# Kernel optimization log

Measured on AMD Instinct MI355X. Metric: run time of the kernel, lower is better.

## Reference

```python
import jax, jax.numpy as jnp
import numpy as np

N, C_F, C_C = 4, 128, 256
H_IMG, W_IMG = 480, 640
HF, WF = H_IMG // 2, W_IMG // 2          # fine feature map 240x320
K, STRIDE, PAD = 5, 4, 2                 # fine_window_size, hw0_f//hw0_c, W//2
WW = K * K                               # 25
L = (H_IMG // 8) * (W_IMG // 8)          # 4800 coarse cells
M = 5000                                 # number of matches
VIEW = (-1, H_IMG * K * 2, WW, W_IMG * K // WW)  # (-1, 4800, 25, 128), exactly the torch .view


def _unfold(x):
    """torch.nn.functional.unfold(x, (K,K), stride=STRIDE, padding=PAD).
    x: [N, C, H, W] -> [N, C*K*K, Ho*Wo] with torch channel ordering (c, kh, kw)."""
    n, c, h, w = x.shape
    xp = jnp.pad(x, ((0, 0), (0, 0), (PAD, PAD), (PAD, PAD)))
    ho = (h + 2 * PAD - K) // STRIDE + 1
    wo = (w + 2 * PAD - K) // STRIDE + 1
    ii = (jnp.arange(ho) * STRIDE)[:, None] + jnp.arange(K)[None, :]  # [Ho, K]
    jj = (jnp.arange(wo) * STRIDE)[:, None] + jnp.arange(K)[None, :]  # [Wo, K]
    p = xp[:, :, ii][:, :, :, :, jj]          # [N, C, Ho, K, Wo, K]
    p = p.transpose(0, 1, 3, 5, 2, 4)          # [N, C, K, K, Ho, Wo]
    return p.reshape(n, c * K * K, ho * wo)


def setup_inputs() -> dict:
    key = jax.random.key(0)
    ks = jax.random.split(key, 11)
    feat_f0 = jax.random.normal(ks[0], (N, C_F, HF, WF), jnp.float32)
    feat_f1 = jax.random.normal(ks[1], (N, C_F, HF, WF), jnp.float32)
    feat_c0 = jax.random.normal(ks[2], (N, L, C_C), jnp.float32)
    feat_c1 = jax.random.normal(ks[3], (N, L, C_C), jnp.float32)
    b_ids = jax.random.randint(ks[4], (M,), 0, N)
    i_ids = jax.random.randint(ks[5], (M,), 0, L)
    j_ids = jax.random.randint(ks[6], (M,), 0, L)
    # kaiming_normal fan_out, relu: std = sqrt(2 / fan_out) with fan_out = out_features
    down_proj_w = jax.random.normal(ks[7], (C_F, C_C), jnp.float32) * np.sqrt(2.0 / C_F)
    down_proj_b = jnp.zeros((C_F,), jnp.float32)
    merge_w = jax.random.normal(ks[8], (C_F, 2 * C_F), jnp.float32) * np.sqrt(2.0 / C_F)
    merge_b = jnp.zeros((C_F,), jnp.float32)
    return {"feat_f0": feat_f0, "feat_f1": feat_f1, "feat_c0": feat_c0, "feat_c1": feat_c1,
            "b_ids": b_ids, "i_ids": i_ids, "j_ids": j_ids,
            "down_proj_w": down_proj_w, "down_proj_b": down_proj_b,
            "merge_w": merge_w, "merge_b": merge_b}


def reference(feat_f0, feat_f1, feat_c0, feat_c1, b_ids, i_ids, j_ids,
              down_proj_w, down_proj_b, merge_w, merge_b):
    # dense unfold (im2col) then faithful memory-reinterpreting .view
    u0 = _unfold(feat_f0).reshape(VIEW)            # [N, 4800, 25, 128]
    u1 = _unfold(feat_f1).reshape(VIEW)
    # sparse window gather
    f0 = u0[b_ids, i_ids]                          # [M, WW, C_F]
    f1 = u1[b_ids, j_ids]                          # [M, WW, C_F]
    # cat_c_feat branch: down-project coarse feats and merge
    c_win = jnp.concatenate([feat_c0[b_ids, i_ids], feat_c1[b_ids, j_ids]], axis=0)  # [2M, C_C]
    c_win = c_win @ down_proj_w.T + down_proj_b                                      # [2M, C_F]
    f = jnp.concatenate([f0, f1], axis=0)                                            # [2M, WW, C_F]
    c_rep = jnp.broadcast_to(c_win[:, None, :], (f.shape[0], WW, C_F))               # [2M, WW, C_F]
    merged = jnp.concatenate([f, c_rep], axis=-1) @ merge_w.T + merge_b              # [2M, WW, C_F]
    return merged[:M], merged[M:]
```

## Files before the change

kernel.cpp:

```cpp
#include <hip/hip_runtime.h>
#include <hip/hip_bf16.h>

#define MM 5000
#define LC 4800

typedef __attribute__((ext_vector_type(8))) short bf16x8;
typedef __attribute__((ext_vector_type(4))) float f32x4;

__device__ __forceinline__ unsigned short f2bf(float f) {
    unsigned int u = __builtin_bit_cast(unsigned int, f);
    u += 0x7fffu + ((u >> 16) & 1u);
    return (unsigned short)(u >> 16);
}

__global__ void k0_prep(const float* __restrict__ merge_w,
                        const float* __restrict__ down_w,
                        const float* __restrict__ merge_b,
                        const float* __restrict__ down_b,
                        unsigned short* __restrict__ w1_bf,
                        unsigned short* __restrict__ wc_bf,
                        float* __restrict__ bvec)
{
    int o = blockIdx.x * 256 + threadIdx.x;
    int cf = o >> 8, cc = o & 255;
    const float* w2row = merge_w + cf * 256 + 128;
    float acc = 0.f;
    #pragma unroll 4
    for (int j = 0; j < 128; ++j)
        acc = fmaf(w2row[j], down_w[j * 256 + cc], acc);
    wc_bf[o] = f2bf(acc);
    if (o < 16384)
        w1_bf[o] = f2bf(merge_w[(o >> 7) * 256 + (o & 127)]);
    if (o < 128) {
        const float* w2r = merge_w + o * 256 + 128;
        float a = merge_b[o];
        for (int j = 0; j < 128; ++j) a = fmaf(down_b[j], w2r[j], a);
        bvec[o] = a;
    }
}

__global__ void __launch_bounds__(256) k1_bias(
    const float* __restrict__ feat_c0, const float* __restrict__ feat_c1,
    const int* __restrict__ b_ids, const int* __restrict__ i_ids,
    const int* __restrict__ j_ids,
    const unsigned short* __restrict__ wc_bf, const float* __restrict__ bvec,
    float* __restrict__ bias2)
{
    __shared__ unsigned short ac[32][264];
    const int t = threadIdx.x;
    const int base = blockIdx.x * 32;
    {
        int row = t >> 3;
        int seg = (t & 7) * 32;
        int sm = base + row; if (sm > 2 * MM - 1) sm = 2 * MM - 1;
        int side = sm >= MM;
        int mm = sm - side * MM;
        int id = side ? j_ids[mm] : i_ids[mm];
        int b  = b_ids[mm];
        const float* src = (side ? feat_c1 : feat_c0)
                           + (size_t)(b * LC + id) * 256 + seg;
        const float4* s4 = (const float4*)src;
        #pragma unroll
        for (int i = 0; i < 8; ++i) {
            float4 v = s4[i];
            ushort4 u; u.x = f2bf(v.x); u.y = f2bf(v.y); u.z = f2bf(v.z); u.w = f2bf(v.w);
            *(ushort4*)&ac[row][seg + i * 4] = u;
        }
    }
    __syncthreads();
    const int lane = t & 63, wave = t >> 6;
    const int ln = lane & 15, q = lane >> 4;
    const int n0 = wave * 32;
    f32x4 acc[2][2] = {};
    #pragma unroll
    for (int k0 = 0; k0 < 8; ++k0) {
        bf16x8 a0 = *(const bf16x8*)&ac[ln][k0 * 32 + q * 8];
        bf16x8 a1 = *(const bf16x8*)&ac[16 + ln][k0 * 32 + q * 8];
        bf16x8 b0 = *(const bf16x8*)(wc_bf + (size_t)(n0 + ln) * 256 + k0 * 32 + q * 8);
        bf16x8 b1 = *(const bf16x8*)(wc_bf + (size_t)(n0 + 16 + ln) * 256 + k0 * 32 + q * 8);
        acc[0][0] = __builtin_amdgcn_mfma_f32_16x16x32_bf16(a0, b0, acc[0][0], 0, 0, 0);
        acc[0][1] = __builtin_amdgcn_mfma_f32_16x16x32_bf16(a0, b1, acc[0][1], 0, 0, 0);
        acc[1][0] = __builtin_amdgcn_mfma_f32_16x16x32_bf16(a1, b0, acc[1][0], 0, 0, 0);
        acc[1][1] = __builtin_amdgcn_mfma_f32_16x16x32_bf16(a1, b1, acc[1][1], 0, 0, 0);
    }
    #pragma unroll
    for (int mt = 0; mt < 2; ++mt)
      #pragma unroll
      for (int nt = 0; nt < 2; ++nt) {
        int cf = n0 + nt * 16 + ln;
        float bv = bvec[cf];
        #pragma unroll
        for (int r = 0; r < 4; ++r) {
            int sm = base + mt * 16 + q * 4 + r;
            if (sm < 2 * MM)
                bias2[(size_t)sm * 128 + cf] = acc[mt][nt][r] + bv;
        }
      }
}

__global__ void __launch_bounds__(256, 6) k2_main(
    const float* __restrict__ feat_f0, const float* __restrict__ feat_f1,
    const int* __restrict__ b_ids, const int* __restrict__ i_ids,
    const int* __restrict__ j_ids,
    const unsigned short* __restrict__ w1_bf, const float* __restrict__ bias2,
    float* __restrict__ out)
{
    __shared__ unsigned short fw[32][136];
    __shared__ float brow[128];
    const int t = threadIdx.x;
    const int bx = blockIdx.x;
    const int side = bx >= MM;
    const int m = bx - side * MM;
    const float* feat = side ? feat_f1 : feat_f0;
    const int l = side ? j_ids[m] : i_ids[m];
    const int n = b_ids[m];
    const float* fn = feat + (size_t)n * (128 * 240 * 320);

    if (t < 128) brow[t] = bias2[(size_t)bx * 128 + t];

    const unsigned fbase = (unsigned)l * 3200u;
    const unsigned cc0 = fbase / 4800u;
    const unsigned p0  = fbase - cc0 * 4800u;
    const unsigned rem = 4800u - p0;
    const int split = (int)(rem < 3200u ? rem : 3200u);
    const unsigned cc1 = cc0 + 1u;
    const int ch0 = (int)(cc0 / 25u), k50 = (int)(cc0 - (unsigned)ch0 * 25u);
    const int kh0 = k50 / 5, kw0 = k50 - kh0 * 5;
    const int ch1 = (int)(cc1 / 25u), k51 = (int)(cc1 - (unsigned)ch1 * 25u);
    const int kh1 = k51 / 5, kw1 = k51 - kh1 * 5;
    const int base0 = ch0 * 76800, base1 = ch1 * 76800;
    const int khm20 = kh0 - 2, khm21 = kh1 - 2;
    const int kwm20 = kw0 - 2, kwm21 = kw1 - 2;

    float val[13];
    unsigned int vmask = 0;
    #pragma unroll
    for (int it = 0; it < 13; ++it) {
        int idx = t + it * 256;
        idx = idx < 3199 ? idx : 3199;
        const int selB = idx >= split;
        const unsigned p = (unsigned)(selB ? idx - split : idx + (int)p0);
        const int ho = (int)(p / 80u);
        const int wo = (int)p - ho * 80;
        const int r   = 4 * ho + (selB ? khm21 : khm20);
        const int col = 4 * wo + (selB ? kwm21 : kwm20);
        const int ok = (r >= 0) & (col >= 0);
        int off = (selB ? base1 : base0) + r * 320 + col;
        off = ok ? off : 0;
        val[it] = fn[off];
        vmask |= (unsigned)ok << it;
    }

    const int lane = t & 63, wave = t >> 6;
    const int ln = lane & 15, q = lane >> 4;
    const int n0 = wave * 32;
    bf16x8 bf[2][4];
    #pragma unroll
    for (int nt = 0; nt < 2; ++nt)
      #pragma unroll
      for (int k0 = 0; k0 < 4; ++k0)
        bf[nt][k0] = *(const bf16x8*)(w1_bf + (n0 + nt * 16 + ln) * 128 + k0 * 32 + q * 8);

    #pragma unroll
    for (int it = 0; it < 13; ++it) {
        int idx = t + it * 256;
        if (it < 12 || idx < 3200) {
            float v = ((vmask >> it) & 1u) ? val[it] : 0.f;
            fw[idx >> 7][idx & 127] = f2bf(v);
        }
    }
    __syncthreads();

    f32x4 acc[2][2] = {};
    #pragma unroll
    for (int k0 = 0; k0 < 4; ++k0) {
        bf16x8 a0 = *(const bf16x8*)&fw[ln][k0 * 32 + q * 8];
        bf16x8 a1 = *(const bf16x8*)&fw[16 + ln][k0 * 32 + q * 8];
        acc[0][0] = __builtin_amdgcn_mfma_f32_16x16x32_bf16(a0, bf[0][k0], acc[0][0], 0, 0, 0);
        acc[0][1] = __builtin_amdgcn_mfma_f32_16x16x32_bf16(a0, bf[1][k0], acc[0][1], 0, 0, 0);
        acc[1][0] = __builtin_amdgcn_mfma_f32_16x16x32_bf16(a1, bf[0][k0], acc[1][0], 0, 0, 0);
        acc[1][1] = __builtin_amdgcn_mfma_f32_16x16x32_bf16(a1, bf[1][k0], acc[1][1], 0, 0, 0);
    }
    float* ob = out + (size_t)bx * 3200;
    #pragma unroll
    for (int nt = 0; nt < 2; ++nt) {
        int cf = n0 + nt * 16 + ln;
        float bv = brow[cf];
        #pragma unroll
        for (int mt = 0; mt < 2; ++mt)
          #pragma unroll
          for (int r = 0; r < 4; ++r) {
            int w = mt * 16 + q * 4 + r;
            if (w < 25)
                ob[w * 128 + cf] = acc[mt][nt][r] + bv;
          }
    }
}

extern "C" void kernel_launch(void* const* d_in, const int* in_sizes, int n_in,
                              void* d_out, int out_size, void* d_ws, size_t ws_size,
                              hipStream_t stream) {
    const float* feat_f0 = (const float*)d_in[0];
    const float* feat_f1 = (const float*)d_in[1];
    const float* feat_c0 = (const float*)d_in[2];
    const float* feat_c1 = (const float*)d_in[3];
    const int*   b_ids   = (const int*)d_in[4];
    const int*   i_ids   = (const int*)d_in[5];
    const int*   j_ids   = (const int*)d_in[6];
    const float* down_w  = (const float*)d_in[7];
    const float* down_b  = (const float*)d_in[8];
    const float* merge_w = (const float*)d_in[9];
    const float* merge_b = (const float*)d_in[10];
    float* out = (float*)d_out;

    char* ws = (char*)d_ws;
    unsigned short* w1_bf = (unsigned short*)(ws);
    unsigned short* wc_bf = (unsigned short*)(ws + 32768);
    float* bvec  = (float*)(ws + 98304);
    float* bias2 = (float*)(ws + 98816);

    hipLaunchKernelGGL(k0_prep, dim3(128), dim3(256), 0, stream,
                       merge_w, down_w, merge_b, down_b, w1_bf, wc_bf, bvec);
    hipLaunchKernelGGL(k1_bias, dim3((2 * MM + 31) / 32), dim3(256), 0, stream,
                       feat_c0, feat_c1, b_ids, i_ids, j_ids, wc_bf, bvec, bias2);
    hipLaunchKernelGGL(k2_main, dim3(2 * MM), dim3(256), 0, stream,
                       feat_f0, feat_f1, b_ids, i_ids, j_ids, w1_bf, bias2, out);
}
```

Baseline: 429.2 us.

## Sort matches by window key and remap block order for cache locality

```diff
diff --git a/kernel.cpp b/kernel.cpp
--- a/kernel.cpp
+++ b/kernel.cpp
@@ -3,6 +3,7 @@
 
 #define MM 5000
 #define LC 4800
+#define NB 38400
 
 typedef __attribute__((ext_vector_type(8))) short bf16x8;
 typedef __attribute__((ext_vector_type(4))) float f32x4;
@@ -19,9 +20,12 @@
                         const float* __restrict__ down_b,
                         unsigned short* __restrict__ w1_bf,
                         unsigned short* __restrict__ wc_bf,
-                        float* __restrict__ bvec)
+                        float* __restrict__ bvec,
+                        unsigned int* __restrict__ hist)
 {
     int o = blockIdx.x * 256 + threadIdx.x;
+    if (o < NB) hist[o] = 0u;
+    if (o + 32768 < NB) hist[o + 32768] = 0u;
     int cf = o >> 8, cc = o & 255;
     const float* w2row = merge_w + cf * 256 + 128;
     float acc = 0.f;
@@ -36,6 +40,64 @@
         float a = merge_b[o];
         for (int j = 0; j < 128; ++j) a = fmaf(down_b[j], w2r[j], a);
         bvec[o] = a;
+    }
+}
+
+__device__ __forceinline__ unsigned sort_key(int s, const int* b_ids,
+                                             const int* i_ids, const int* j_ids) {
+    int side = s >= MM;
+    int mm = s - side * MM;
+    int l = side ? j_ids[mm] : i_ids[mm];
+    return (unsigned)(side * (4 * LC) + b_ids[mm] * LC + l);
+}
+
+__global__ void k_hist(const int* __restrict__ b_ids, const int* __restrict__ i_ids,
+                       const int* __restrict__ j_ids, unsigned int* __restrict__ hist)
+{
+    int s = blockIdx.x * 256 + threadIdx.x;
+    if (s < 2 * MM)
+        atomicAdd(&hist[sort_key(s, b_ids, i_ids, j_ids)], 1u);
+}
+
+__global__ void __launch_bounds__(1024) k_scan(unsigned int* __restrict__ hist)
+{
+    __shared__ unsigned part[1024];
+    const int t = threadIdx.x;
+    const int CH = (NB + 1023) / 1024;
+    const int s0 = t * CH;
+    unsigned loc[CH];
+    unsigned sum = 0;
+    #pragma unroll
+    for (int i = 0; i < CH; ++i) {
+        int idx = s0 + i;
+        unsigned v = (idx < NB) ? hist[idx] : 0u;
+        loc[i] = sum;
+        sum += v;
+    }
+    part[t] = sum;
+    __syncthreads();
+    for (int off = 1; off < 1024; off <<= 1) {
+        unsigned v = (t >= off) ? part[t - off] : 0u;
+        __syncthreads();
+        part[t] += v;
+        __syncthreads();
+    }
+    unsigned base = (t == 0) ? 0u : part[t - 1];
+    #pragma unroll
+    for (int i = 0; i < CH; ++i) {
+        int idx = s0 + i;
+        if (idx < NB) hist[idx] = base + loc[i];
+    }
+}
+
+__global__ void k_scatter(const int* __restrict__ b_ids, const int* __restrict__ i_ids,
+                          const int* __restrict__ j_ids, unsigned int* __restrict__ hist,
+                          int* __restrict__ perm)
+{
+    int s = blockIdx.x * 256 + threadIdx.x;
+    if (s < 2 * MM) {
+        unsigned pos = atomicAdd(&hist[sort_key(s, b_ids, i_ids, j_ids)], 1u);
+        perm[pos] = s;
     }
 }
 
@@ -103,12 +165,14 @@
     const int* __restrict__ b_ids, const int* __restrict__ i_ids,
     const int* __restrict__ j_ids,
     const unsigned short* __restrict__ w1_bf, const float* __restrict__ bias2,
+    const int* __restrict__ perm,
     float* __restrict__ out)
 {
     __shared__ unsigned short fw[32][136];
     __shared__ float brow[128];
     const int t = threadIdx.x;
-    const int bx = blockIdx.x;
+    const int bid = blockIdx.x;
+    const int bx = perm[(bid & 7) * 1250 + (bid >> 3)];
     const int side = bx >= MM;
     const int m = bx - side * MM;
     const float* feat = side ? feat_f1 : feat_f0;
@@ -218,11 +282,18 @@
     unsigned short* wc_bf = (unsigned short*)(ws + 32768);
     float* bvec  = (float*)(ws + 98304);
     float* bias2 = (float*)(ws + 98816);
+    int*   perm  = (int*)(ws + 5218816);
+    unsigned int* hist = (unsigned int*)(ws + 5258816);
 
     hipLaunchKernelGGL(k0_prep, dim3(128), dim3(256), 0, stream,
-                       merge_w, down_w, merge_b, down_b, w1_bf, wc_bf, bvec);
+                       merge_w, down_w, merge_b, down_b, w1_bf, wc_bf, bvec, hist);
+    hipLaunchKernelGGL(k_hist, dim3(40), dim3(256), 0, stream,
+                       b_ids, i_ids, j_ids, hist);
+    hipLaunchKernelGGL(k_scan, dim3(1), dim3(1024), 0, stream, hist);
+    hipLaunchKernelGGL(k_scatter, dim3(40), dim3(256), 0, stream,
+                       b_ids, i_ids, j_ids, hist, perm);
     hipLaunchKernelGGL(k1_bias, dim3((2 * MM + 31) / 32), dim3(256), 0, stream,
                        feat_c0, feat_c1, b_ids, i_ids, j_ids, wc_bf, bvec, bias2);
     hipLaunchKernelGGL(k2_main, dim3(2 * MM), dim3(256), 0, stream,
-                       feat_f0, feat_f1, b_ids, i_ids, j_ids, w1_bf, bias2, out);
-}
+                       feat_f0, feat_f1, b_ids, i_ids, j_ids, w1_bf, bias2, perm, out);
+}
```

Measured after the change: 461.4 us. 1.07x slower.

## Sort matches by window key to improve gather locality; stage stores through LDS

Applied to the files above, without the earlier changes.

```diff
diff --git a/kernel.cpp b/kernel.cpp
--- a/kernel.cpp
+++ b/kernel.cpp
@@ -36,6 +36,61 @@
         float a = merge_b[o];
         for (int j = 0; j < 128; ++j) a = fmaf(down_b[j], w2r[j], a);
         bvec[o] = a;
+    }
+}
+
+__global__ void __launch_bounds__(1024) k_sort(
+    const int* __restrict__ b_ids, const int* __restrict__ i_ids,
+    const int* __restrict__ j_ids, int* __restrict__ perm)
+{
+    __shared__ unsigned hist[4800];
+    __shared__ unsigned part[1024];
+    const int t = threadIdx.x;
+    for (int i = t; i < 4800; i += 1024) hist[i] = 0u;
+    __syncthreads();
+    unsigned key[10];
+    #pragma unroll
+    for (int i = 0; i < 10; ++i) {
+        int s = t + i * 1024;
+        if (s < 2 * MM) {
+            int side = s >= MM;
+            int mm = s - side * MM;
+            int l = side ? j_ids[mm] : i_ids[mm];
+            key[i] = (unsigned)(side * (4 * LC) + b_ids[mm] * LC + l) >> 3;
+            atomicAdd(&hist[key[i]], 1u);
+        } else key[i] = 0u;
+    }
+    __syncthreads();
+    unsigned loc[5], sum = 0u;
+    #pragma unroll
+    for (int i = 0; i < 5; ++i) {
+        int idx = t * 5 + i;
+        unsigned v = (idx < 4800) ? hist[idx] : 0u;
+        loc[i] = sum; sum += v;
+    }
+    part[t] = sum;
+    __syncthreads();
+    for (int off = 1; off < 1024; off <<= 1) {
+        unsigned v = (t >= off) ? part[t - off] : 0u;
+        __syncthreads();
+        part[t] += v;
+        __syncthreads();
+    }
+    unsigned base = (t == 0) ? 0u : part[t - 1];
+    __syncthreads();
+    #pragma unroll
+    for (int i = 0; i < 5; ++i) {
+        int idx = t * 5 + i;
+        if (idx < 4800) hist[idx] = base + loc[i];
+    }
+    __syncthreads();
+    #pragma unroll
+    for (int i = 0; i < 10; ++i) {
+        int s = t + i * 1024;
+        if (s < 2 * MM) {
+            unsigned pos = atomicAdd(&hist[key[i]], 1u);
+            perm[pos] = s;
+        }
     }
 }
 
@@ -98,17 +153,22 @@
       }
 }
 
-__global__ void __launch_bounds__(256, 6) k2_main(
+__global__ void __launch_bounds__(256, 8) k2_main(
     const float* __restrict__ feat_f0, const float* __restrict__ feat_f1,
     const int* __restrict__ b_ids, const int* __restrict__ i_ids,
     const int* __restrict__ j_ids,
     const unsigned short* __restrict__ w1_bf, const float* __restrict__ bias2,
+    const int* __restrict__ perm,
     float* __restrict__ out)
 {
-    __shared__ unsigned short fw[32][136];
-    __shared__ float brow[128];
+    __shared__ char smem[12800];
+    unsigned short (*fw)[136] = (unsigned short (*)[136])smem;
+    float* brow = (float*)(smem + 8704);
+    float* dls  = (float*)smem;
+
     const int t = threadIdx.x;
-    const int bx = blockIdx.x;
+    const int bid = blockIdx.x;
+    const int bx = perm[(bid & 7) * 1250 + (bid >> 3)];
     const int side = bx >= MM;
     const int m = bx - side * MM;
     const float* feat = side ? feat_f1 : feat_f0;
@@ -171,6 +231,9 @@
     }
     __syncthreads();
 
+    const float bv0 = brow[n0 + ln];
+    const float bv1 = brow[n0 + 16 + ln];
+
     f32x4 acc[2][2] = {};
     #pragma unroll
     for (int k0 = 0; k0 < 4; ++k0) {
@@ -181,20 +244,28 @@
         acc[1][0] = __builtin_amdgcn_mfma_f32_16x16x32_bf16(a1, bf[0][k0], acc[1][0], 0, 0, 0);
         acc[1][1] = __builtin_amdgcn_mfma_f32_16x16x32_bf16(a1, bf[1][k0], acc[1][1], 0, 0, 0);
     }
-    float* ob = out + (size_t)bx * 3200;
+    __syncthreads();
+
     #pragma unroll
     for (int nt = 0; nt < 2; ++nt) {
         int cf = n0 + nt * 16 + ln;
-        float bv = brow[cf];
+        float bv = nt ? bv1 : bv0;
         #pragma unroll
         for (int mt = 0; mt < 2; ++mt)
           #pragma unroll
           for (int r = 0; r < 4; ++r) {
             int w = mt * 16 + q * 4 + r;
             if (w < 25)
-                ob[w * 128 + cf] = acc[mt][nt][r] + bv;
+                dls[w * 128 + cf] = acc[mt][nt][r] + bv;
           }
     }
+    __syncthreads();
+
+    float4* ob4 = (float4*)(out + (size_t)bx * 3200);
+    const float4* d4 = (const float4*)dls;
+    #pragma unroll
+    for (int i = t; i < 800; i += 256)
+        ob4[i] = d4[i];
 }
 
 extern "C" void kernel_launch(void* const* d_in, const int* in_sizes, int n_in,
@@ -218,11 +289,14 @@
     unsigned short* wc_bf = (unsigned short*)(ws + 32768);
     float* bvec  = (float*)(ws + 98304);
     float* bias2 = (float*)(ws + 98816);
+    int*   perm  = (int*)(ws + 5218816);
 
     hipLaunchKernelGGL(k0_prep, dim3(128), dim3(256), 0, stream,
                        merge_w, down_w, merge_b, down_b, w1_bf, wc_bf, bvec);
+    hipLaunchKernelGGL(k_sort, dim3(1), dim3(1024), 0, stream,
+                       b_ids, i_ids, j_ids, perm);
     hipLaunchKernelGGL(k1_bias, dim3((2 * MM + 31) / 32), dim3(256), 0, stream,
                        feat_c0, feat_c1, b_ids, i_ids, j_ids, wc_bf, bvec, bias2);
     hipLaunchKernelGGL(k2_main, dim3(2 * MM), dim3(256), 0, stream,
-                       feat_f0, feat_f1, b_ids, i_ids, j_ids, w1_bf, bias2, out);
-}
+                       feat_f0, feat_f1, b_ids, i_ids, j_ids, w1_bf, bias2, perm, out);
+}
```

New measurement: 430.1 us. Within noise of the previous version (+0.2%).

## Sort window gathers by location and pair them per block with duplicate reuse

Applied to the files above, without the earlier changes.

```diff
diff --git a/kernel.cpp b/kernel.cpp
--- a/kernel.cpp
+++ b/kernel.cpp
@@ -44,10 +44,55 @@
     const int* __restrict__ b_ids, const int* __restrict__ i_ids,
     const int* __restrict__ j_ids,
     const unsigned short* __restrict__ wc_bf, const float* __restrict__ bvec,
-    float* __restrict__ bias2)
+    float* __restrict__ bias2, int* __restrict__ perm)
 {
-    __shared__ unsigned short ac[32][264];
+    __shared__ unsigned smbuf_u[5056];
     const int t = threadIdx.x;
+
+    if (blockIdx.x == (2 * MM + 31) / 32) {
+        unsigned* hist = smbuf_u;
+        unsigned* part = smbuf_u + 4800;
+        for (int i = t; i < 4800; i += 256) hist[i] = 0u;
+        __syncthreads();
+        for (int s = t; s < 2 * MM; s += 256) {
+            int side = s >= MM; int mm = s - side * MM;
+            int l = side ? j_ids[mm] : i_ids[mm];
+            atomicAdd(&hist[((unsigned)(side * (4 * LC) + b_ids[mm] * LC + l)) >> 3], 1u);
+        }
+        __syncthreads();
+        unsigned loc[19], sum = 0u;
+        const int s0i = t * 19;
+        #pragma unroll
+        for (int i = 0; i < 19; ++i) {
+            int idx = s0i + i;
+            unsigned v = (idx < 4800) ? hist[idx] : 0u;
+            loc[i] = sum; sum += v;
+        }
+        part[t] = sum;
+        __syncthreads();
+        for (int off = 1; off < 256; off <<= 1) {
+            unsigned v = (t >= off) ? part[t - off] : 0u;
+            __syncthreads();
+            part[t] += v;
+            __syncthreads();
+        }
+        unsigned base = (t == 0) ? 0u : part[t - 1];
+        #pragma unroll
+        for (int i = 0; i < 19; ++i) {
+            int idx = s0i + i;
+            if (idx < 4800) hist[idx] = base + loc[i];
+        }
+        __syncthreads();
+        for (int s = t; s < 2 * MM; s += 256) {
+            int side = s >= MM; int mm = s - side * MM;
+            int l = side ? j_ids[mm] : i_ids[mm];
+            unsigned pos = atomicAdd(&hist[((unsigned)(side * (4 * LC) + b_ids[mm] * LC + l)) >> 3], 1u);
+            perm[pos] = s;
+        }
+        return;
+    }
+
+    unsigned short (*ac)[264] = (unsigned short (*)[264])smbuf_u;
     const int base = blockIdx.x * 32;
     {
         int row = t >> 3;
@@ -98,69 +143,51 @@
       }
 }
 
-__global__ void __launch_bounds__(256, 6) k2_main(
-    const float* __restrict__ feat_f0, const float* __restrict__ feat_f1,
-    const int* __restrict__ b_ids, const int* __restrict__ i_ids,
-    const int* __restrict__ j_ids,
-    const unsigned short* __restrict__ w1_bf, const float* __restrict__ bias2,
-    float* __restrict__ out)
-{
-    __shared__ unsigned short fw[32][136];
-    __shared__ float brow[128];
-    const int t = threadIdx.x;
-    const int bx = blockIdx.x;
-    const int side = bx >= MM;
-    const int m = bx - side * MM;
-    const float* feat = side ? feat_f1 : feat_f0;
-    const int l = side ? j_ids[m] : i_ids[m];
-    const int n = b_ids[m];
-    const float* fn = feat + (size_t)n * (128 * 240 * 320);
-
-    if (t < 128) brow[t] = bias2[(size_t)bx * 128 + t];
-
-    const unsigned fbase = (unsigned)l * 3200u;
-    const unsigned cc0 = fbase / 4800u;
-    const unsigned p0  = fbase - cc0 * 4800u;
-    const unsigned rem = 4800u - p0;
-    const int split = (int)(rem < 3200u ? rem : 3200u);
-    const unsigned cc1 = cc0 + 1u;
-    const int ch0 = (int)(cc0 / 25u), k50 = (int)(cc0 - (unsigned)ch0 * 25u);
-    const int kh0 = k50 / 5, kw0 = k50 - kh0 * 5;
-    const int ch1 = (int)(cc1 / 25u), k51 = (int)(cc1 - (unsigned)ch1 * 25u);
-    const int kh1 = k51 / 5, kw1 = k51 - kh1 * 5;
-    const int base0 = ch0 * 76800, base1 = ch1 * 76800;
-    const int khm20 = kh0 - 2, khm21 = kh1 - 2;
-    const int kwm20 = kw0 - 2, kwm21 = kw1 - 2;
-
-    float val[13];
-    unsigned int vmask = 0;
+struct GP { int split, base0, base1, khm20, khm21, kwm20, kwm21, p0; };
+
+__device__ __forceinline__ GP decodeParams(int l) {
+    GP g;
+    unsigned fbase = (unsigned)l * 3200u;
+    unsigned cc0 = fbase / 4800u;
+    unsigned p0 = fbase - cc0 * 4800u;
+    unsigned rem = 4800u - p0;
+    g.split = (int)(rem < 3200u ? rem : 3200u);
+    g.p0 = (int)p0;
+    unsigned cc1 = cc0 + 1u;
+    int ch0 = (int)(cc0 / 25u), k50 = (int)(cc0 - (unsigned)ch0 * 25u);
+    int kh0 = k50 / 5, kw0 = k50 - kh0 * 5;
+    int ch1 = (int)(cc1 / 25u), k51 = (int)(cc1 - (unsigned)ch1 * 25u);
+    int kh1 = k51 / 5, kw1 = k51 - kh1 * 5;
+    g.base0 = ch0 * 76800; g.base1 = ch1 * 76800;
+    g.khm20 = kh0 - 2; g.khm21 = kh1 - 2;
+    g.kwm20 = kw0 - 2; g.kwm21 = kw1 - 2;
+    return g;
+}
+
+__device__ __forceinline__ unsigned gatherIssue(const GP g, const float* __restrict__ fn,
+                                                int t, float val[13]) {
+    unsigned vmask = 0;
     #pragma unroll
     for (int it = 0; it < 13; ++it) {
         int idx = t + it * 256;
         idx = idx < 3199 ? idx : 3199;
-        const int selB = idx >= split;
-        const unsigned p = (unsigned)(selB ? idx - split : idx + (int)p0);
+        const int selB = idx >= g.split;
+        const unsigned p = (unsigned)(selB ? idx - g.split : idx + g.p0);
         const int ho = (int)(p / 80u);
         const int wo = (int)p - ho * 80;
-        const int r   = 4 * ho + (selB ? khm21 : khm20);
-        const int col = 4 * wo + (selB ? kwm21 : kwm20);
+        const int r   = 4 * ho + (selB ? g.khm21 : g.khm20);
+        const int col = 4 * wo + (selB ? g.kwm21 : g.kwm20);
         const int ok = (r >= 0) & (col >= 0);
-        int off = (selB ? base1 : base0) + r * 320 + col;
+        int off = (selB ? g.base1 : g.base0) + r * 320 + col;
         off = ok ? off : 0;
         val[it] = fn[off];
         vmask |= (unsigned)ok << it;
     }
-
-    const int lane = t & 63, wave = t >> 6;
-    const int ln = lane & 15, q = lane >> 4;
-    const int n0 = wave * 32;
-    bf16x8 bf[2][4];
-    #pragma unroll
-    for (int nt = 0; nt < 2; ++nt)
-      #pragma unroll
-      for (int k0 = 0; k0 < 4; ++k0)
-        bf[nt][k0] = *(const bf16x8*)(w1_bf + (n0 + nt * 16 + ln) * 128 + k0 * 32 + q * 8);
-
+    return vmask;
+}
+
+__device__ __forceinline__ void cvtToLds(unsigned short (*fw)[136], int t,
+                                         const float val[13], unsigned vmask) {
     #pragma unroll
     for (int it = 0; it < 13; ++it) {
         int idx = t + it * 256;
@@ -169,9 +196,11 @@
             fw[idx >> 7][idx & 127] = f2bf(v);
         }
     }
-    __syncthreads();
-
-    f32x4 acc[2][2] = {};
+}
+
+__device__ __forceinline__ void mfma22(const unsigned short (*fw)[136],
+                                       const bf16x8 (&bf)[2][4],
+                                       int ln, int q, f32x4 (&acc)[2][2]) {
     #pragma unroll
     for (int k0 = 0; k0 < 4; ++k0) {
         bf16x8 a0 = *(const bf16x8*)&fw[ln][k0 * 32 + q * 8];
@@ -181,6 +210,11 @@
         acc[1][0] = __builtin_amdgcn_mfma_f32_16x16x32_bf16(a1, bf[0][k0], acc[1][0], 0, 0, 0);
         acc[1][1] = __builtin_amdgcn_mfma_f32_16x16x32_bf16(a1, bf[1][k0], acc[1][1], 0, 0, 0);
     }
+}
+
+__device__ __forceinline__ void storeD(const f32x4 (&acc)[2][2], const float* brow,
+                                       float* __restrict__ out, int bx,
+                                       int n0, int ln, int q) {
     float* ob = out + (size_t)bx * 3200;
     #pragma unroll
     for (int nt = 0; nt < 2; ++nt) {
@@ -195,6 +229,76 @@
                 ob[w * 128 + cf] = acc[mt][nt][r] + bv;
           }
     }
+}
+
+__global__ void __launch_bounds__(256, 6) k2_main(
+    const float* __restrict__ feat_f0, const float* __restrict__ feat_f1,
+    const int* __restrict__ b_ids, const int* __restrict__ i_ids,
+    const int* __restrict__ j_ids,
+    const unsigned short* __restrict__ w1_bf, const float* __restrict__ bias2,
+    const int* __restrict__ perm,
+    float* __restrict__ out)
+{
+    __shared__ unsigned short fw0[32][136];
+    __shared__ unsigned short fw1[32][136];
+    __shared__ float brow0[128], brow1[128];
+    const int t = threadIdx.x;
+    const int bid = blockIdx.x;
+    const int qq = (bid & 7) * 625 + (bid >> 3);
+    const int s0 = perm[2 * qq], s1 = perm[2 * qq + 1];
+
+    const int side0 = s0 >= MM, m0 = s0 - side0 * MM;
+    const int l0 = side0 ? j_ids[m0] : i_ids[m0];
+    const int n0b = b_ids[m0];
+    const int side1 = s1 >= MM, m1 = s1 - side1 * MM;
+    const int l1 = side1 ? j_ids[m1] : i_ids[m1];
+    const int n1b = b_ids[m1];
+    const float* fn0 = (side0 ? feat_f1 : feat_f0) + (size_t)n0b * (128 * 240 * 320);
+    const float* fn1 = (side1 ? feat_f1 : feat_f0) + (size_t)n1b * (128 * 240 * 320);
+    const bool dup = (l0 == l1) && (n0b == n1b) && (side0 == side1);
+
+    if (t < 128) {
+        brow0[t] = bias2[(size_t)s0 * 128 + t];
+        brow1[t] = bias2[(size_t)s1 * 128 + t];
+    }
+
+    GP g0 = decodeParams(l0);
+    float val[13];
+    unsigned vm = gatherIssue(g0, fn0, t, val);
+
+    const int lane = t & 63, wave = t >> 6;
+    const int ln = lane & 15, q = lane >> 4;
+    const int n0 = wave * 32;
+    bf16x8 bf[2][4];
+    #pragma unroll
+    for (int nt = 0; nt < 2; ++nt)
+      #pragma unroll
+      for (int k0 = 0; k0 < 4; ++k0)
+        bf[nt][k0] = *(const bf16x8*)(w1_bf + (n0 + nt * 16 + ln) * 128 + k0 * 32 + q * 8);
+
+    cvtToLds(fw0, t, val, vm);
+    __syncthreads();
+
+    unsigned vm1 = 0;
+    if (!dup) {
+        GP g1 = decodeParams(l1);
+        vm1 = gatherIssue(g1, fn1, t, val);
+    }
+
+    f32x4 acc[2][2] = {};
+    mfma22(fw0, bf, ln, q, acc);
+    storeD(acc, brow0, out, s0, n0, ln, q);
+    if (dup) {
+        storeD(acc, brow1, out, s1, n0, ln, q);
+        return;
+    }
+
+    cvtToLds(fw1, t, val, vm1);
+    __syncthreads();
+
+    f32x4 acc1[2][2] = {};
+    mfma22(fw1, bf, ln, q, acc1);
+    storeD(acc1, brow1, out, s1, n0, ln, q);
 }
 
 extern "C" void kernel_launch(void* const* d_in, const int* in_sizes, int n_in,
@@ -218,11 +322,12 @@
     unsigned short* wc_bf = (unsigned short*)(ws + 32768);
     float* bvec  = (float*)(ws + 98304);
     float* bias2 = (float*)(ws + 98816);
+    int*   perm  = (int*)(ws + 5218816);
 
     hipLaunchKernelGGL(k0_prep, dim3(128), dim3(256), 0, stream,
                        merge_w, down_w, merge_b, down_b, w1_bf, wc_bf, bvec);
-    hipLaunchKernelGGL(k1_bias, dim3((2 * MM + 31) / 32), dim3(256), 0, stream,
-                       feat_c0, feat_c1, b_ids, i_ids, j_ids, wc_bf, bvec, bias2);
-    hipLaunchKernelGGL(k2_main, dim3(2 * MM), dim3(256), 0, stream,
-                       feat_f0, feat_f1, b_ids, i_ids, j_ids, w1_bf, bias2, out);
-}
+    hipLaunchKernelGGL(k1_bias, dim3((2 * MM + 31) / 32 + 1), dim3(256), 0, stream,
+                       feat_c0, feat_c1, b_ids, i_ids, j_ids, wc_bf, bvec, bias2, perm);
+    hipLaunchKernelGGL(k2_main, dim3(MM), dim3(256), 0, stream,
+                       feat_f0, feat_f1, b_ids, i_ids, j_ids, w1_bf, bias2, perm, out);
+}
```

New measurement: 464.8 us. 1.08x slower.
